# Performance work log

Hardware: AMD Instinct MI355X
Metric: run time of the kernel (lower is better)

Reference implementation:

```python
import jax, jax.numpy as jnp
import numpy as np

TEMPERATURE = 8.0  # sqrt(head_dim=64)


def sparsemax(z):
    """Sparsemax along the last axis (Martins & Astudillo 2016)."""
    S = z.shape[-1]
    z_sorted = -jnp.sort(-z, axis=-1)            # descending sort
    cs = jnp.cumsum(z_sorted, axis=-1)
    ks = jnp.arange(1, S + 1, dtype=z.dtype)
    support = 1.0 + ks * z_sorted > cs           # entries in the support set
    k_sup = jnp.sum(support, axis=-1, keepdims=True)  # support size >= 1
    tau = (jnp.take_along_axis(cs, k_sup - 1, axis=-1) - 1.0) / k_sup.astype(z.dtype)
    return jnp.maximum(z - tau, 0.0)


def setup_inputs() -> dict:
    key = jax.random.key(0)
    kq, kk, kv, km = jax.random.split(key, 4)
    B, Lq, Lk, D = 64, 1024, 1024, 64
    q = jax.random.normal(kq, (B, Lq, D), dtype=jnp.float32)
    k = jax.random.normal(kk, (B, Lk, D), dtype=jnp.float32)
    v = jax.random.normal(kv, (B, Lk, D), dtype=jnp.float32)
    mask = jax.random.randint(km, (B, Lq, Lk), 0, 2).astype(bool)  # True = masked out
    return {"q": q, "k": k, "v": v, "mask": mask}


def reference(q, k, v, mask):
    # scores: [B, Lq, Lk]
    attn = jnp.einsum('bqd,bkd->bqk', q / TEMPERATURE, k)
    # mask out disallowed keys with -inf
    attn = jnp.where(mask, -jnp.inf, attn)
    # rows where ALL keys are masked: set scores to 0 (avoids NaN in sparsemax)
    inf_mask = jnp.all(mask, axis=2, keepdims=True)  # [B, Lq, 1]
    attn = jnp.where(inf_mask, 0.0, attn)
    attn = sparsemax(attn)
    # zero out fully-masked rows again (dropout has p=0.0 -> identity in eval)
    attn = jnp.where(inf_mask, 0.0, attn)
    out = jnp.einsum('bqk,bkd->bqd', attn, v)
    return (out, attn)
```

## Files before the change

### kernel.cpp

```cpp
#include <hip/hip_runtime.h>
#include <float.h>


#define BATCH    64
#define SEQQ     1024
#define SEQK     1024
#define DHEAD    64

typedef short short8 __attribute__((ext_vector_type(8)));
typedef float f32x4  __attribute__((ext_vector_type(4)));

__device__ __forceinline__ unsigned short bf16_rne(float f) {
    unsigned u = __float_as_uint(f);
    u += 0x7fffu + ((u >> 16) & 1u);
    return (unsigned short)(u >> 16);
}

__device__ __forceinline__ void cvt_hilo8(const float* fv, float scale,
                                          short8* hi, short8* lo) {
    #pragma unroll
    for (int j = 0; j < 8; ++j) {
        float f = fv[j] * scale;
        unsigned short hb = bf16_rne(f);
        float hf = __uint_as_float((unsigned)hb << 16);
        (*hi)[j] = (short)hb;
        (*lo)[j] = (short)bf16_rne(f - hf);
    }
}

__global__ void detect_mask_fmt(const unsigned char* __restrict__ m,
                                int* __restrict__ flag) {
    __shared__ int s_found;
    if (threadIdx.x == 0) s_found = 0;
    __syncthreads();
    int found = 0;
    for (int o = threadIdx.x; o < 65536; o += 256) {
        if ((o & 3) != 0 && m[o] != 0) found = 1;
    }
    if (found) atomicOr(&s_found, 1);
    __syncthreads();
    if (threadIdx.x == 0) *flag = s_found;
}

__global__ __launch_bounds__(256) void score_kernel(
        const float* __restrict__ q, const float* __restrict__ k,
        unsigned short* __restrict__ sbuf, int pitch) {
    const int lane = threadIdx.x & 63;
    const int wave = threadIdx.x >> 6;
    const int quad = lane >> 4;
    const int l15  = lane & 15;
    const int qt = blockIdx.x >> 6;
    const int b  = blockIdx.x & 63;

    __shared__ unsigned short klds[2 * 128 * 64];

    const float* qrow =
        q + ((size_t)b * SEQQ + qt * 64 + wave * 16 + l15) * DHEAD;
    short8 a_hi[2], a_lo[2];
    #pragma unroll
    for (int kc = 0; kc < 2; ++kc) {
        const float4* src = (const float4*)(qrow + kc * 32 + quad * 8);
        float4 f0 = src[0], f1 = src[1];
        float fv[8] = {f0.x, f0.y, f0.z, f0.w, f1.x, f1.y, f1.z, f1.w};
        cvt_hilo8(fv, 0.125f, &a_hi[kc], &a_lo[kc]);
    }

    const float* kb = k + (size_t)b * SEQK * DHEAD;
    unsigned short* srow0 =
        sbuf + ((size_t)b * SEQQ + qt * 64 + wave * 16) * (size_t)pitch;

    for (int kt = 0; kt < 8; ++kt) {
        __syncthreads();
        const float* kbase = kb + (size_t)kt * 128 * DHEAD;
        #pragma unroll
        for (int it = 0; it < 4; ++it) {
            int e   = threadIdx.x + 256 * it;
            int key = e >> 3, db = e & 7;
            const float4* src = (const float4*)(kbase + key * DHEAD + db * 8);
            float4 f0 = src[0], f1 = src[1];
            float fv[8] = {f0.x, f0.y, f0.z, f0.w, f1.x, f1.y, f1.z, f1.w};
            short8 hi, lo;
            cvt_hilo8(fv, 1.0f, &hi, &lo);
            int off = key * 64 + ((db ^ (key & 7)) * 8);
            *(short8*)(klds + off)        = hi;
            *(short8*)(klds + 8192 + off) = lo;
        }
        __syncthreads();

        unsigned short* srow = srow0 + kt * 128;
        #pragma unroll
        for (int g = 0; g < 8; ++g) {
            int key = g * 16 + l15;
            short8 b_hi[2], b_lo[2];
            #pragma unroll
            for (int kc = 0; kc < 2; ++kc) {
                int db  = kc * 4 + quad;
                int off = key * 64 + ((db ^ (key & 7)) * 8);
                b_hi[kc] = *(const short8*)(klds + off);
                b_lo[kc] = *(const short8*)(klds + 8192 + off);
            }
            f32x4 acc = {0.f, 0.f, 0.f, 0.f};
            #pragma unroll
            for (int kc = 0; kc < 2; ++kc) {
                acc = __builtin_amdgcn_mfma_f32_16x16x32_bf16(a_hi[kc], b_hi[kc], acc, 0, 0, 0);
                acc = __builtin_amdgcn_mfma_f32_16x16x32_bf16(a_lo[kc], b_hi[kc], acc, 0, 0, 0);
                acc = __builtin_amdgcn_mfma_f32_16x16x32_bf16(a_hi[kc], b_lo[kc], acc, 0, 0, 0);
            }
            #pragma unroll
            for (int r = 0; r < 4; ++r)
                srow[(size_t)(quad * 4 + r) * (size_t)pitch + g * 16 + l15] =
                    bf16_rne(acc[r]);
        }
    }
}

__global__ __launch_bounds__(256) void sparsemax_pv(
        const float* __restrict__ v, const void* __restrict__ mask,
        const int* __restrict__ fmt_flag,
        float* __restrict__ out, float* __restrict__ attn,
        const unsigned short* __restrict__ sbuf, int pitch) {
    const int lane = threadIdx.x & 63;
    const int wave = threadIdx.x >> 6;
    const int row  = blockIdx.x * 4 + wave;
    const int b    = row >> 10;
    float* arow = attn + (size_t)row * SEQK;
    const int mask_is_byte = fmt_flag ? *fmt_flag : 1;

    __shared__ float pbuf[4][SEQK];

    const ushort4* s4 =
        (const ushort4*)(sbuf + (size_t)row * (size_t)pitch);
    float s[16];
    #pragma unroll
    for (int t = 0; t < 4; ++t) {
        ushort4 u = s4[lane + 64 * t];
        s[4*t+0] = __uint_as_float((unsigned)u.x << 16);
        s[4*t+1] = __uint_as_float((unsigned)u.y << 16);
        s[4*t+2] = __uint_as_float((unsigned)u.z << 16);
        s[4*t+3] = __uint_as_float((unsigned)u.w << 16);
    }
    if (mask_is_byte) {
        const unsigned* m32 =
            (const unsigned*)((const unsigned char*)mask + (size_t)row * SEQK);
        #pragma unroll
        for (int t = 0; t < 4; ++t) {
            unsigned m = m32[lane + 64 * t];
            if (m & 0x000000ffu) s[4*t+0] = -FLT_MAX;
            if (m & 0x0000ff00u) s[4*t+1] = -FLT_MAX;
            if (m & 0x00ff0000u) s[4*t+2] = -FLT_MAX;
            if (m & 0xff000000u) s[4*t+3] = -FLT_MAX;
        }
    } else {
        const int4* m4 = (const int4*)((const int*)mask + (size_t)row * SEQK);
        #pragma unroll
        for (int t = 0; t < 4; ++t) {
            int4 m = m4[lane + 64 * t];
            if (m.x) s[4*t+0] = -FLT_MAX;
            if (m.y) s[4*t+1] = -FLT_MAX;
            if (m.z) s[4*t+2] = -FLT_MAX;
            if (m.w) s[4*t+3] = -FLT_MAX;
        }
    }

    float mx = -FLT_MAX;
    #pragma unroll
    for (int i = 0; i < 16; ++i) mx = fmaxf(mx, s[i]);
    #pragma unroll
    for (int off = 32; off >= 1; off >>= 1)
        mx = fmaxf(mx, __shfl_xor(mx, off, 64));

    if (mx <= -FLT_MAX) {
        f32x4 z = {0.f, 0.f, 0.f, 0.f};
        #pragma unroll
        for (int t = 0; t < 4; ++t)
            __builtin_nontemporal_store(z, (f32x4*)arow + lane + 64 * t);
        out[(size_t)row * DHEAD + lane] = 0.f;
        return;
    }

    float thr = mx - 1.0f, tau = 0.f;
    int cnt_prev = -1;
    for (int it = 0; it < 32; ++it) {
        float lsum = 0.f; int lcnt = 0;
        #pragma unroll
        for (int i = 0; i < 16; ++i)
            if (s[i] > thr) { lsum += s[i]; lcnt++; }
        #pragma unroll
        for (int off = 32; off >= 1; off >>= 1) {
            lsum += __shfl_xor(lsum, off, 64);
            lcnt += __shfl_xor(lcnt, off, 64);
        }
        tau = (lsum - 1.0f) / (float)lcnt;
        if (lcnt == cnt_prev) break;
        cnt_prev = lcnt;
        thr = tau;
    }

    float p[16];
    #pragma unroll
    for (int i = 0; i < 16; ++i) {
        float pv = s[i] - tau;
        p[i] = pv > 0.f ? pv : 0.f;
    }
    #pragma unroll
    for (int t = 0; t < 4; ++t) {
        f32x4 f = {p[4*t+0], p[4*t+1], p[4*t+2], p[4*t+3]};
        __builtin_nontemporal_store(f, (f32x4*)arow + lane + 64 * t);
        *(f32x4*)&pbuf[wave][4 * (lane + 64 * t)] = f;
    }

    const float* vbase = v + (size_t)b * SEQK * DHEAD;
    float oacc = 0.f;
    #pragma unroll
    for (int t = 0; t < 4; ++t) {
        #pragma unroll
        for (int c = 0; c < 4; ++c) {
            int i = 4 * t + c;
            unsigned long long mb = __ballot(p[i] > 0.f);
            while (mb) {
                int k0, k1 = -1, k2 = -1, k3 = -1;
                k0 = __ffsll(mb) - 1; mb &= mb - 1;
                if (mb) { k1 = __ffsll(mb) - 1; mb &= mb - 1; }
                if (mb) { k2 = __ffsll(mb) - 1; mb &= mb - 1; }
                if (mb) { k3 = __ffsll(mb) - 1; mb &= mb - 1; }
                int key0 = 4 * k0 + 256 * t + c;
                float pj0 = pbuf[wave][key0];
                float v0  = vbase[(size_t)key0 * DHEAD + lane];
                float pj1 = 0.f, pj2 = 0.f, pj3 = 0.f;
                float v1 = 0.f, v2 = 0.f, v3 = 0.f;
                if (k1 >= 0) {
                    int key1 = 4 * k1 + 256 * t + c;
                    pj1 = pbuf[wave][key1];
                    v1  = vbase[(size_t)key1 * DHEAD + lane];
                }
                if (k2 >= 0) {
                    int key2 = 4 * k2 + 256 * t + c;
                    pj2 = pbuf[wave][key2];
                    v2  = vbase[(size_t)key2 * DHEAD + lane];
                }
                if (k3 >= 0) {
                    int key3 = 4 * k3 + 256 * t + c;
                    pj3 = pbuf[wave][key3];
                    v3  = vbase[(size_t)key3 * DHEAD + lane];
                }
                oacc = fmaf(pj0, v0, oacc);
                if (k1 >= 0) oacc = fmaf(pj1, v1, oacc);
                if (k2 >= 0) oacc = fmaf(pj2, v2, oacc);
                if (k3 >= 0) oacc = fmaf(pj3, v3, oacc);
            }
        }
    }
    out[(size_t)row * DHEAD + lane] = oacc;
}

extern "C" void kernel_launch(void* const* d_in, const int* in_sizes, int n_in,
                              void* d_out, int out_size, void* d_ws, size_t ws_size,
                              hipStream_t stream) {
    const float* q = (const float*)d_in[0];
    const float* k = (const float*)d_in[1];
    const float* v = (const float*)d_in[2];
    const void*  m = d_in[3];

    float* out  = (float*)d_out;
    float* attn = out + (size_t)BATCH * SEQQ * DHEAD;

    int* flag = nullptr;
    if (ws_size >= sizeof(int)) {
        flag = (int*)d_ws;
        detect_mask_fmt<<<1, 256, 0, stream>>>((const unsigned char*)m, flag);
    }

    const size_t s_elems = (size_t)BATCH * SEQQ * SEQK;
    unsigned short* sbuf;
    int pitch;
    if (ws_size >= 16 + s_elems * sizeof(unsigned short)) {
        sbuf  = (unsigned short*)d_ws + 8;
        pitch = SEQK;
    } else {
        sbuf  = (unsigned short*)attn;
        pitch = 2 * SEQK;
    }

    score_kernel<<<(SEQQ / 64) * BATCH, 256, 0, stream>>>(q, k, sbuf, pitch);

    sparsemax_pv<<<(BATCH * SEQQ) / 4, 256, 0, stream>>>(
        v, m, flag, out, attn, sbuf, pitch);
}
```

Before: 682.3 us.

## Precompute bf16 hi/lo K tiles and stream them into LDS via direct-to-LDS loads

A new prep kernel converts K once per batch into swizzled bf16 hi/lo tiles in workspace. The score kernel then fills LDS with global_load_lds DMA instead of having each of the 16 query-tile blocks per batch redo the fp32-to-bf16 split. This removes redundant conversion work and register staging, at the cost of an extra kernel launch and extra workspace traffic. The sparsemax kernel's score and mask reads also become nontemporal loads to limit cache pollution.

```diff
diff --git a/kernel.cpp b/kernel.cpp
--- a/kernel.cpp
+++ b/kernel.cpp
@@ -9,6 +9,11 @@
 
 typedef short short8 __attribute__((ext_vector_type(8)));
 typedef float f32x4  __attribute__((ext_vector_type(4)));
+typedef unsigned short us4v __attribute__((ext_vector_type(4)));
+
+typedef const __attribute__((address_space(1))) unsigned int as1_cuint;
+typedef __attribute__((address_space(3))) unsigned int as3_uint;
+typedef __attribute__((address_space(3))) unsigned char as3_uchar;
 
 __device__ __forceinline__ unsigned short bf16_rne(float f) {
     unsigned u = __float_as_uint(f);
@@ -42,7 +47,99 @@
     if (threadIdx.x == 0) *flag = s_found;
 }
 
-__global__ __launch_bounds__(256) void score_kernel(
+__global__ __launch_bounds__(256) void kprep(
+        const float* __restrict__ k, unsigned short* __restrict__ kbuf) {
+    int gid  = blockIdx.x * 256 + threadIdx.x;
+    int db   = gid & 7;
+    int keyg = (gid >> 3) & 1023;
+    int b    = gid >> 13;
+    int kt   = keyg >> 7;
+    int key  = keyg & 127;
+
+    const float4* src =
+        (const float4*)(k + ((size_t)b * SEQK + keyg) * DHEAD + db * 8);
+    float4 f0 = src[0], f1 = src[1];
+    float fv[8] = {f0.x, f0.y, f0.z, f0.w, f1.x, f1.y, f1.z, f1.w};
+    short8 hi, lo;
+    cvt_hilo8(fv, 1.0f, &hi, &lo);
+
+    unsigned short* tile = kbuf + (size_t)(b * 8 + kt) * 16384;
+    int off = key * 64 + ((db ^ (key & 7)) * 8);
+    *(short8*)(tile + off)        = hi;
+    *(short8*)(tile + 8192 + off) = lo;
+}
+
+__global__ __launch_bounds__(256) void score_kernel_dma(
+        const float* __restrict__ q, const unsigned short* __restrict__ kbuf,
+        unsigned short* __restrict__ sbuf, int pitch) {
+    const int lane = threadIdx.x & 63;
+    const int wave = threadIdx.x >> 6;
+    const int quad = lane >> 4;
+    const int l15  = lane & 15;
+    const int qt = blockIdx.x >> 6;
+    const int b  = blockIdx.x & 63;
+
+    __shared__ unsigned short klds[2 * 128 * 64];
+
+    const float* qrow =
+        q + ((size_t)b * SEQQ + qt * 64 + wave * 16 + l15) * DHEAD;
+    short8 a_hi[2], a_lo[2];
+    #pragma unroll
+    for (int kc = 0; kc < 2; ++kc) {
+        const float4* src = (const float4*)(qrow + kc * 32 + quad * 8);
+        float4 f0 = src[0], f1 = src[1];
+        float fv[8] = {f0.x, f0.y, f0.z, f0.w, f1.x, f1.y, f1.z, f1.w};
+        cvt_hilo8(fv, 0.125f, &a_hi[kc], &a_lo[kc]);
+    }
+
+    unsigned short* srow0 =
+        sbuf + ((size_t)b * SEQQ + qt * 64 + wave * 16) * (size_t)pitch;
+
+    for (int kt = 0; kt < 8; ++kt) {
+        __syncthreads();
+        const unsigned char* gtile =
+            (const unsigned char*)(kbuf + (size_t)(b * 8 + kt) * 16384);
+        {
+            unsigned base = wave * 8192 + lane * 16;
+            #pragma unroll
+            for (int j = 0; j < 8; ++j) {
+                unsigned off = base + j * 1024;
+                as1_cuint* gp = (as1_cuint*)(gtile + off);
+                as3_uint*  lp = (as3_uint*)((as3_uchar*)klds +
+                                            (wave * 8192 + j * 1024));
+                __builtin_amdgcn_global_load_lds(gp, lp, 16, 0, 0);
+            }
+        }
+        __syncthreads();
+
+        unsigned short* srow = srow0 + kt * 128;
+        #pragma unroll
+        for (int g = 0; g < 8; ++g) {
+            int key = g * 16 + l15;
+            short8 b_hi[2], b_lo[2];
+            #pragma unroll
+            for (int kc = 0; kc < 2; ++kc) {
+                int db  = kc * 4 + quad;
+                int off = key * 64 + ((db ^ (key & 7)) * 8);
+                b_hi[kc] = *(const short8*)(klds + off);
+                b_lo[kc] = *(const short8*)(klds + 8192 + off);
+            }
+            f32x4 acc = {0.f, 0.f, 0.f, 0.f};
+            #pragma unroll
+            for (int kc = 0; kc < 2; ++kc) {
+                acc = __builtin_amdgcn_mfma_f32_16x16x32_bf16(a_hi[kc], b_hi[kc], acc, 0, 0, 0);
+                acc = __builtin_amdgcn_mfma_f32_16x16x32_bf16(a_lo[kc], b_hi[kc], acc, 0, 0, 0);
+                acc = __builtin_amdgcn_mfma_f32_16x16x32_bf16(a_hi[kc], b_lo[kc], acc, 0, 0, 0);
+            }
+            #pragma unroll
+            for (int r = 0; r < 4; ++r)
+                srow[(size_t)(quad * 4 + r) * (size_t)pitch + g * 16 + l15] =
+                    bf16_rne(acc[r]);
+        }
+    }
+}
+
+__global__ __launch_bounds__(256) void score_kernel_cvt(
         const float* __restrict__ q, const float* __restrict__ k,
         unsigned short* __restrict__ sbuf, int pitch) {
     const int lane = threadIdx.x & 63;
@@ -128,37 +225,39 @@
 
     __shared__ float pbuf[4][SEQK];
 
-    const ushort4* s4 =
-        (const ushort4*)(sbuf + (size_t)row * (size_t)pitch);
+    const us4v* s4 = (const us4v*)(sbuf + (size_t)row * (size_t)pitch);
     float s[16];
     #pragma unroll
     for (int t = 0; t < 4; ++t) {
-        ushort4 u = s4[lane + 64 * t];
-        s[4*t+0] = __uint_as_float((unsigned)u.x << 16);
-        s[4*t+1] = __uint_as_float((unsigned)u.y << 16);
-        s[4*t+2] = __uint_as_float((unsigned)u.z << 16);
-        s[4*t+3] = __uint_as_float((unsigned)u.w << 16);
+        us4v u = __builtin_nontemporal_load(s4 + lane + 64 * t);
+        s[4*t+0] = __uint_as_float((unsigned)u[0] << 16);
+        s[4*t+1] = __uint_as_float((unsigned)u[1] << 16);
+        s[4*t+2] = __uint_as_float((unsigned)u[2] << 16);
+        s[4*t+3] = __uint_as_float((unsigned)u[3] << 16);
     }
     if (mask_is_byte) {
         const unsigned* m32 =
             (const unsigned*)((const unsigned char*)mask + (size_t)row * SEQK);
         #pragma unroll
         for (int t = 0; t < 4; ++t) {
-            unsigned m = m32[lane + 64 * t];
+            unsigned m = __builtin_nontemporal_load(m32 + lane + 64 * t);
             if (m & 0x000000ffu) s[4*t+0] = -FLT_MAX;
             if (m & 0x0000ff00u) s[4*t+1] = -FLT_MAX;
             if (m & 0x00ff0000u) s[4*t+2] = -FLT_MAX;
             if (m & 0xff000000u) s[4*t+3] = -FLT_MAX;
         }
     } else {
-        const int4* m4 = (const int4*)((const int*)mask + (size_t)row * SEQK);
+        const int* mi = (const int*)mask + (size_t)row * SEQK;
         #pragma unroll
         for (int t = 0; t < 4; ++t) {
-            int4 m = m4[lane + 64 * t];
-            if (m.x) s[4*t+0] = -FLT_MAX;
-            if (m.y) s[4*t+1] = -FLT_MAX;
-            if (m.z) s[4*t+2] = -FLT_MAX;
-            if (m.w) s[4*t+3] = -FLT_MAX;
+            int m0 = __builtin_nontemporal_load(mi + 4 * (lane + 64 * t) + 0);
+            int m1 = __builtin_nontemporal_load(mi + 4 * (lane + 64 * t) + 1);
+            int m2 = __builtin_nontemporal_load(mi + 4 * (lane + 64 * t) + 2);
+            int m3 = __builtin_nontemporal_load(mi + 4 * (lane + 64 * t) + 3);
+            if (m0) s[4*t+0] = -FLT_MAX;
+            if (m1) s[4*t+1] = -FLT_MAX;
+            if (m2) s[4*t+2] = -FLT_MAX;
+            if (m3) s[4*t+3] = -FLT_MAX;
         }
     }
 
@@ -270,10 +369,13 @@
         detect_mask_fmt<<<1, 256, 0, stream>>>((const unsigned char*)m, flag);
     }
 
-    const size_t s_elems = (size_t)BATCH * SEQQ * SEQK;
+    const size_t S_BYTES = (size_t)BATCH * SEQQ * SEQK * 2;
+    const size_t K_BYTES = (size_t)BATCH * SEQK * DHEAD * 2 * 2;
+
     unsigned short* sbuf;
     int pitch;
-    if (ws_size >= 16 + s_elems * sizeof(unsigned short)) {
+    bool s_in_ws = ws_size >= 16 + S_BYTES;
+    if (s_in_ws) {
         sbuf  = (unsigned short*)d_ws + 8;
         pitch = SEQK;
     } else {
@@ -281,7 +383,17 @@
         pitch = 2 * SEQK;
     }
 
-    score_kernel<<<(SEQQ / 64) * BATCH, 256, 0, stream>>>(q, k, sbuf, pitch);
+    bool k_in_ws = s_in_ws && ws_size >= 16 + S_BYTES + K_BYTES;
+    if (k_in_ws) {
+        unsigned short* kbuf =
+            (unsigned short*)((char*)d_ws + 16 + S_BYTES);
+        kprep<<<(BATCH * SEQK * 8) / 256, 256, 0, stream>>>(k, kbuf);
+        score_kernel_dma<<<(SEQQ / 64) * BATCH, 256, 0, stream>>>(
+            q, kbuf, sbuf, pitch);
+    } else {
+        score_kernel_cvt<<<(SEQQ / 64) * BATCH, 256, 0, stream>>>(
+            q, k, sbuf, pitch);
+    }
 
     sparsemax_pv<<<(BATCH * SEQQ) / 4, 256, 0, stream>>>(
         v, m, flag, out, attn, sbuf, pitch);
```

Result: faster. 646.2 us (-5.3%).
